# Performance work log

Hardware: AMD Instinct MI355X
Metric: run time of the kernel (lower is better)

## Reference

```python
import jax, jax.numpy as jnp
import numpy as np

D_K = 766  # feature dim, also softmax temperature per module init
NEG = -1000000000.0


def setup_inputs() -> dict:
    key = jax.random.key(0)
    k1, k2, k3 = jax.random.split(key, 3)
    B, H, L, D = 2, 4, 2048, D_K
    Q = jax.random.normal(k1, (B, H, L, D), dtype=jnp.float32)
    K = jax.random.normal(k2, (B, H, L, D), dtype=jnp.float32)
    attn_mask = jax.random.randint(k3, (B, H, L, L), 0, 2) > 0  # bool [B,H,Lk,Lq]
    return {"Q": Q, "K": K, "attn_mask": attn_mask}


def reference(Q, K, attn_mask):
    # scores: [B,H,Lq,Lk]
    scores = jnp.einsum("bhqd,bhkd->bhqk", Q, K) / np.sqrt(D_K).astype(np.float32)
    # mask is [B,H,Lk,Lq]; torch applies mask.transpose(2,3)
    scores = jnp.where(jnp.swapaxes(attn_mask, 2, 3), NEG, scores)
    attn1 = jax.nn.softmax(scores, axis=-1)                       # row softmax
    attn2 = jax.nn.softmax(jnp.swapaxes(scores, -1, -2), axis=-1)  # col softmax
    # dropout prob = 0.0 -> identity
    context1 = jnp.einsum("bhqk,bhkd->bhqd", attn1, K)
    context2 = jnp.einsum("bhkq,bhqd->bhkd", attn2, Q)
    return (context1, context2, attn1, attn2)
```

## Files before the change

kernel.cpp:

```cpp
#include <hip/hip_runtime.h>
#include <math.h>

#define L 2048
#define DK 766
#define DKP 768
#define NBH 8
#define NR (NBH * L)
#define NEGV -1000000000.0f

typedef __attribute__((ext_vector_type(8))) short bf16x8_t;
typedef __attribute__((ext_vector_type(4))) float f32x4_t;

#define LDT 72

typedef __attribute__((address_space(1))) const unsigned int gu32;
typedef __attribute__((address_space(3))) unsigned int lu32;

__device__ __forceinline__ short f2bf(float x) {
    union { float f; unsigned u; } v;
    v.f = x;
    unsigned r = v.u + 0x7fff + ((v.u >> 16) & 1);
    return (short)(r >> 16);
}

__device__ __forceinline__ float bf2f(short s) {
    union { unsigned u; float f; } v;
    v.u = ((unsigned)(unsigned short)s) << 16;
    return v.f;
}

__device__ __forceinline__ void gl_lds16(const void* g, void* l) {
    __builtin_amdgcn_global_load_lds((gu32*)g, (lu32*)l, 16, 0, 0);
}

#define BARR() asm volatile("s_barrier" ::: "memory")
#define VMW() asm volatile("s_waitcnt vmcnt(0)" ::: "memory")
#define PRIO1() __builtin_amdgcn_s_setprio(1)
#define PRIO0() __builtin_amdgcn_s_setprio(0)

__global__ __launch_bounds__(256) void k_cvtT(const float* __restrict__ Q,
                                              const float* __restrict__ K,
                                              short* __restrict__ Qb,
                                              short* __restrict__ Kb,
                                              short* __restrict__ Qt,
                                              short* __restrict__ Kt) {
    __shared__ short T[64 * LDT];
    const int tz = blockIdx.z;
    const int bh = tz & 7;
    const float* X = (tz < 8) ? Q : K;
    short* Xb = (tz < 8) ? Qb : Kb;
    short* Xt = (tz < 8) ? Qt : Kt;
    X += (size_t)bh * L * DK;
    Xb += (size_t)bh * L * DKP;
    Xt += (size_t)bh * DKP * L;
    const int r0 = blockIdx.y * 64, c0 = blockIdx.x * 64;
    const int t = threadIdx.x;
    const int rl = t >> 2, cc = (t & 3) * 16;

    bf16x8_t v0, v1;
#pragma unroll
    for (int p = 0; p < 8; ++p) {
        int c = c0 + cc + 2 * p;
        float2 f = (c < DK) ? *(const float2*)&X[(size_t)(r0 + rl) * DK + c]
                            : make_float2(0.f, 0.f);
        if (p < 4) { v0[2 * p] = f2bf(f.x); v0[2 * p + 1] = f2bf(f.y); }
        else { v1[2 * (p - 4)] = f2bf(f.x); v1[2 * (p - 4) + 1] = f2bf(f.y); }
    }
    *(bf16x8_t*)&Xb[(size_t)(r0 + rl) * DKP + c0 + cc] = v0;
    *(bf16x8_t*)&Xb[(size_t)(r0 + rl) * DKP + c0 + cc + 8] = v1;
    *(bf16x8_t*)&T[rl * LDT + cc] = v0;
    *(bf16x8_t*)&T[rl * LDT + cc + 8] = v1;
    __syncthreads();
    bf16x8_t w0, w1;
#pragma unroll
    for (int p = 0; p < 8; ++p) {
        w0[p] = T[(cc + p) * LDT + rl];
        w1[p] = T[(cc + 8 + p) * LDT + rl];
    }
    *(bf16x8_t*)&Xt[(size_t)(c0 + rl) * L + r0 + cc] = w0;
    *(bf16x8_t*)&Xt[(size_t)(c0 + rl) * L + r0 + cc + 8] = w1;
}

__global__ __launch_bounds__(256) void k_scoresT(const short* __restrict__ Kb,
                                                 const short* __restrict__ Qb,
                                                 const int* __restrict__ mask,
                                                 short* __restrict__ Sb,
                                                 float* __restrict__ prowM,
                                                 float* __restrict__ prowS,
                                                 float* __restrict__ pcolM,
                                                 float* __restrict__ pcolS) {
    __shared__ __align__(16) short As[128 * 64];
    __shared__ __align__(16) short Bs[128 * 64];
    int flat = blockIdx.x + (blockIdx.y << 4) + (blockIdx.z << 8);
    int nw = (flat & 7) * 256 + (flat >> 3);
    const int bxp = nw & 15;
    const int byp = (nw >> 4) & 15;
    const int bh = nw >> 8;

    const short* Am = Kb + (size_t)bh * L * DKP;
    const short* Bm = Qb + (size_t)bh * L * DKP;
    const int* Mm = mask + (size_t)bh * L * L;
    short* Sm = Sb + (size_t)bh * L * L;
    const int m0 = byp * 128, n0 = bxp * 128;
    const int t = threadIdx.x, lane = t & 63, wid = t >> 6;
    const int wm = (wid >> 1) * 64, wn = (wid & 1) * 64;
    const int lr = lane & 15, lg = lane >> 4;
    const int lrow = lane >> 3, lcol = lane & 7;

    f32x4_t acc[4][4];
#pragma unroll
    for (int i = 0; i < 4; ++i)
#pragma unroll
        for (int j = 0; j < 4; ++j) acc[i][j] = f32x4_t{0.f, 0.f, 0.f, 0.f};

    for (int k0 = 0; k0 < DKP; k0 += 64) {
#pragma unroll
        for (int g = 0; g < 4; ++g) {
            int row = wid * 32 + g * 8 + lrow;
            gl_lds16(&Am[(size_t)(m0 + row) * DKP + k0 + lcol * 8],
                     (char*)As + wid * 4096 + g * 1024);
            gl_lds16(&Bm[(size_t)(n0 + row) * DKP + k0 + lcol * 8],
                     (char*)Bs + wid * 4096 + g * 1024);
        }
        __syncthreads();
#pragma unroll
        for (int ks = 0; ks < 2; ++ks) {
            bf16x8_t av[4], bv[4];
#pragma unroll
            for (int i = 0; i < 4; ++i)
                av[i] = *(bf16x8_t*)&As[(wm + i * 16 + lr) * 64 + ks * 32 + lg * 8];
#pragma unroll
            for (int j = 0; j < 4; ++j)
                bv[j] = *(bf16x8_t*)&Bs[(wn + j * 16 + lr) * 64 + ks * 32 + lg * 8];
#pragma unroll
            for (int i = 0; i < 4; ++i)
#pragma unroll
                for (int j = 0; j < 4; ++j)
                    acc[i][j] = __builtin_amdgcn_mfma_f32_16x16x32_bf16(
                        av[i], bv[j], acc[i][j], 0, 0, 0);
        }
        __syncthreads();
    }

    const float scale = 1.0f / sqrtf((float)DK);
#pragma unroll
    for (int i = 0; i < 4; ++i) {
        int krow = m0 + wm + i * 16 + lg * 4;
#pragma unroll
        for (int j = 0; j < 4; ++j) {
            int qcol = n0 + wn + j * 16 + lr;
#pragma unroll
            for (int r = 0; r < 4; ++r) {
                int mv = Mm[(size_t)(krow + r) * L + qcol];
                float v = mv ? NEGV : acc[i][j][r] * scale;
                acc[i][j][r] = v;
                Sm[(size_t)(krow + r) * L + qcol] = f2bf(v);
            }
        }
    }

    float* redb = (float*)As;
#pragma unroll
    for (int i = 0; i < 4; ++i) {
#pragma unroll
        for (int r = 0; r < 4; ++r) {
            float rm = fmaxf(fmaxf(acc[i][0][r], acc[i][1][r]),
                             fmaxf(acc[i][2][r], acc[i][3][r]));
#pragma unroll
            for (int m = 1; m < 16; m <<= 1) rm = fmaxf(rm, __shfl_xor(rm, m, 64));
            float rs = 0.f;
#pragma unroll
            for (int j = 0; j < 4; ++j) rs += expf(acc[i][j][r] - rm);
#pragma unroll
            for (int m = 1; m < 16; m <<= 1) rs += __shfl_xor(rs, m, 64);
            if (lr == 0) {
                int row = wm + i * 16 + lg * 4 + r;
                redb[(wid & 1) * 128 + row] = rm;
                redb[256 + (wid & 1) * 128 + row] = rs;
            }
        }
    }
#pragma unroll
    for (int j = 0; j < 4; ++j) {
        float cm = -INFINITY;
#pragma unroll
        for (int i = 0; i < 4; ++i)
#pragma unroll
            for (int r = 0; r < 4; ++r) cm = fmaxf(cm, acc[i][j][r]);
        cm = fmaxf(cm, __shfl_xor(cm, 16, 64));
        cm = fmaxf(cm, __shfl_xor(cm, 32, 64));
        float cs = 0.f;
#pragma unroll
        for (int i = 0; i < 4; ++i)
#pragma unroll
            for (int r = 0; r < 4; ++r) cs += expf(acc[i][j][r] - cm);
        cs += __shfl_xor(cs, 16, 64);
        cs += __shfl_xor(cs, 32, 64);
        if (lg == 0) {
            int col = wn + j * 16 + lr;
            redb[512 + (wid >> 1) * 128 + col] = cm;
            redb[768 + (wid >> 1) * 128 + col] = cs;
        }
    }
    __syncthreads();
    if (t < 128) {
        float mA = redb[t], mB = redb[128 + t];
        float sA = redb[256 + t], sB = redb[256 + 128 + t];
        float mm = fmaxf(mA, mB);
        float ss = sA * expf(mA - mm) + sB * expf(mB - mm);
        size_t o = (size_t)bxp * NR + bh * L + m0 + t;
        prowM[o] = mm;
        prowS[o] = ss;
    } else {
        int c = t - 128;
        float mA = redb[512 + c], mB = redb[512 + 128 + c];
        float sA = redb[768 + c], sB = redb[768 + 128 + c];
        float mm = fmaxf(mA, mB);
        float ss = sA * expf(mA - mm) + sB * expf(mB - mm);
        size_t o = (size_t)byp * NR + bh * L + n0 + c;
        pcolM[o] = mm;
        pcolS[o] = ss;
    }
}

__global__ __launch_bounds__(256) void k_comb16(const float* __restrict__ prowM,
                                                const float* __restrict__ prowS,
                                                const float* __restrict__ pcolM,
                                                const float* __restrict__ pcolS,
                                                float* __restrict__ m1,
                                                float* __restrict__ r1,
                                                float* __restrict__ m2,
                                                float* __restrict__ r2) {
    int idx = blockIdx.x * 256 + threadIdx.x;
    float m = -INFINITY;
#pragma unroll
    for (int c = 0; c < 16; ++c) m = fmaxf(m, prowM[(size_t)c * NR + idx]);
    float s = 0.f;
#pragma unroll
    for (int c = 0; c < 16; ++c)
        s += prowS[(size_t)c * NR + idx] * expf(prowM[(size_t)c * NR + idx] - m);
    m2[idx] = m;
    r2[idx] = 1.0f / s;

    m = -INFINITY;
#pragma unroll
    for (int c = 0; c < 16; ++c) m = fmaxf(m, pcolM[(size_t)c * NR + idx]);
    s = 0.f;
#pragma unroll
    for (int c = 0; c < 16; ++c)
        s += pcolS[(size_t)c * NR + idx] * expf(pcolM[(size_t)c * NR + idx] - m);
    m1[idx] = m;
    r1[idx] = 1.0f / s;
}

__global__ __launch_bounds__(256) void k_apply(const short* __restrict__ Sb,
                                               const float* __restrict__ mr,
                                               const float* __restrict__ rr,
                                               const float* __restrict__ mc,
                                               const float* __restrict__ rc,
                                               float* __restrict__ OutIn,
                                               float* __restrict__ OutTr,
                                               short* __restrict__ bIn,
                                               short* __restrict__ bTr) {
    __shared__ float T[64][65];
    const int bh = blockIdx.z;
    const int rb0 = blockIdx.x * 64, cb0 = blockIdx.y * 64;
    const short* Sm = Sb + (size_t)bh * L * L;
    float* Oin = OutIn + (size_t)bh * L * L;
    float* Otr = OutTr + (size_t)bh * L * L;
    const int t = threadIdx.x, tx = t & 15, ty = t >> 4;

    float4 mcv = *(const float4*)&mc[bh * L + cb0 + tx * 4];
    float4 rcv = *(const float4*)&rc[bh * L + cb0 + tx * 4];

#pragma unroll
    for (int i = 0; i < 4; ++i) {
        int r = rb0 + ty * 4 + i;
        float mrv = mr[bh * L + r], rrv = rr[bh * L + r];
        short4 sx = *(const short4*)&Sm[(size_t)r * L + cb0 + tx * 4];
        float x0 = bf2f(sx.x), x1 = bf2f(sx.y), x2 = bf2f(sx.z), x3 = bf2f(sx.w);
        float4 e = make_float4(expf(x0 - mrv) * rrv, expf(x1 - mrv) * rrv,
                               expf(x2 - mrv) * rrv, expf(x3 - mrv) * rrv);
        *(float4*)&Oin[(size_t)r * L + cb0 + tx * 4] = e;
        short4 b = make_short4(f2bf(e.x), f2bf(e.y), f2bf(e.z), f2bf(e.w));
        *(short4*)&bIn[(size_t)bh * L * L + (size_t)r * L + cb0 + tx * 4] = b;
        T[tx * 4 + 0][ty * 4 + i] = expf(x0 - mcv.x) * rcv.x;
        T[tx * 4 + 1][ty * 4 + i] = expf(x1 - mcv.y) * rcv.y;
        T[tx * 4 + 2][ty * 4 + i] = expf(x2 - mcv.z) * rcv.z;
        T[tx * 4 + 3][ty * 4 + i] = expf(x3 - mcv.w) * rcv.w;
    }
    __syncthreads();
#pragma unroll
    for (int i = 0; i < 4; ++i) {
        int c = ty * 4 + i;
        float4 v = make_float4(T[c][tx * 4], T[c][tx * 4 + 1], T[c][tx * 4 + 2],
                               T[c][tx * 4 + 3]);
        *(float4*)&Otr[(size_t)(cb0 + c) * L + rb0 + tx * 4] = v;
        short4 b = make_short4(f2bf(v.x), f2bf(v.y), f2bf(v.z), f2bf(v.w));
        *(short4*)&bTr[(size_t)bh * L * L + (size_t)(cb0 + c) * L + rb0 + tx * 4] = b;
    }
}

__global__ __launch_bounds__(512, 2) void k_ctx8(const short* __restrict__ a1b,
                                                 const short* __restrict__ a2b,
                                                 const short* __restrict__ Kt,
                                                 const short* __restrict__ Qt,
                                                 float* __restrict__ c1,
                                                 float* __restrict__ c2) {
    __shared__ __align__(16) short LB[57344];

    int flat = blockIdx.x;
    int nw = (flat & 7) * 64 + (flat >> 3);
    int inst = nw >> 5, rem = nw & 31;
    int myp = rem >> 2, nxp = rem & 3;
    int bh = inst & 7;
    const short* Am = ((inst < 8) ? a1b : a2b) + (size_t)bh * L * L;
    const short* Bt = ((inst < 8) ? Kt : Qt) + (size_t)bh * DKP * L;
    float* Cm = ((inst < 8) ? c1 : c2) + (size_t)bh * L * DK;
    const int m0 = myp * 256, n0 = nxp * 192;

    const int t = threadIdx.x, lane = t & 63, wid = t >> 6;
    const int wr = wid >> 2, wc = wid & 3;
    const int lr = lane & 15, lg = lane >> 4;

    const int schunk = (lane & 7) ^ (lane >> 3);
    const short* aSrc = Am + (size_t)(m0 + wid * 8 + (lane >> 3)) * L + schunk * 8;
    const short* bSrc = Bt + (size_t)(n0 + wid * 8 + (lane >> 3)) * L + schunk * 8;
    char* ldsA = (char*)LB;
    char* ldsB = (char*)LB + 65536;

#define STAGEA(cb, k0n)                                                               \
    do {                                                                              \
        gl_lds16(aSrc + (k0n), ldsA + (cb)*32768 + wid * 1024);                       \
        gl_lds16(aSrc + (size_t)64 * L + (k0n), ldsA + (cb)*32768 + 8192 + wid * 1024); \
        gl_lds16(aSrc + (size_t)128 * L + (k0n), ldsA + (cb)*32768 + 16384 + wid * 1024); \
        gl_lds16(aSrc + (size_t)192 * L + (k0n), ldsA + (cb)*32768 + 24576 + wid * 1024); \
    } while (0)
#define STAGEB(cb, k0n)                                                               \
    do {                                                                              \
        gl_lds16(bSrc + (k0n), ldsB + (cb)*24576 + wid * 1024);                       \
        gl_lds16(bSrc + (size_t)64 * L + (k0n), ldsB + (cb)*24576 + 8192 + wid * 1024); \
        gl_lds16(bSrc + (size_t)128 * L + (k0n), ldsB + (cb)*24576 + 16384 + wid * 1024); \
    } while (0)

    const int axr = lr & 7;
    const int kc0 = ((0 + lg) ^ axr) * 8;
    const int kc1 = ((4 + lg) ^ axr) * 8;
    const int aRd = wr * 8192 + lr * 64;
    const int bRd = 32768 + (wc * 48 + lr) * 64;

#define LDA0(c, i) (*(const bf16x8_t*)&LB[(c)*16384 + aRd + (i)*1024 + kc0])
#define LDA1(c, i) (*(const bf16x8_t*)&LB[(c)*16384 + aRd + (i)*1024 + kc1])
#define LDB0(c, j) (*(const bf16x8_t*)&LB[bRd + (c)*12288 + (j)*1024 + kc0])
#define LDB1(c, j) (*(const bf16x8_t*)&LB[bRd + (c)*12288 + (j)*1024 + kc1])

    f32x4_t acc[8][3];
#pragma unroll
    for (int i = 0; i < 8; ++i)
#pragma unroll
        for (int j = 0; j < 3; ++j) acc[i][j] = f32x4_t{0.f, 0.f, 0.f, 0.f};

    bf16x8_t bfr[3][2];

#define PHASE(c, i0, EXTRA)                                                           \
    do {                                                                              \
        bf16x8_t a00 = LDA0(c, i0), a01 = LDA1(c, i0);                                \
        bf16x8_t a10 = LDA0(c, (i0) + 1), a11 = LDA1(c, (i0) + 1);                    \
        EXTRA;                                                                        \
        BARR();                                                                       \
        PRIO1();                                                                      \
        _Pragma("unroll") for (int j = 0; j < 3; ++j) {                               \
            acc[i0][j] = __builtin_amdgcn_mfma_f32_16x16x32_bf16(a00, bfr[j][0],      \
                                                                 acc[i0][j], 0, 0, 0); \
            acc[i0][j] = __builtin_amdgcn_mfma_f32_16x16x32_bf16(a01, bfr[j][1],      \
                                                                 acc[i0][j], 0, 0, 0); \
            acc[(i0) + 1][j] = __builtin_amdgcn_mfma_f32_16x16x32_bf16(               \
                a10, bfr[j][0], acc[(i0) + 1][j], 0, 0, 0);                           \
            acc[(i0) + 1][j] = __builtin_amdgcn_mfma_f32_16x16x32_bf16(               \
                a11, bfr[j][1], acc[(i0) + 1][j], 0, 0, 0);                           \
        }                                                                             \
        PRIO0();                                                                      \
    } while (0)

    const int NT = L / 64;
    STAGEA(0, 0);
    STAGEB(0, 0);
    VMW();
    BARR();

    for (int kt = 0; kt < NT; ++kt) {
        const int c = kt & 1;
        const bool ds = (kt + 1 < NT);
        const int k0n = (kt + 1) * 64;
#pragma unroll
        for (int j = 0; j < 3; ++j) {
            bfr[j][0] = LDB0(c, j);
            bfr[j][1] = LDB1(c, j);
        }
        PHASE(c, 0, if (ds) STAGEA(c ^ 1, k0n));
        BARR();
        PHASE(c, 2, if (ds) STAGEB(c ^ 1, k0n));
        BARR();
        PHASE(c, 4, ((void)0));
        BARR();
        PHASE(c, 6, ((void)0));
        if (ds) VMW();
        BARR();
    }

#pragma unroll
    for (int i = 0; i < 8; ++i) {
        int row = m0 + wr * 128 + i * 16 + lg * 4;
#pragma unroll
        for (int j = 0; j < 3; ++j) {
            int col = n0 + wc * 48 + j * 16 + lr;
            if (col < DK) {
#pragma unroll
                for (int r = 0; r < 4; ++r)
                    Cm[(size_t)(row + r) * DK + col] = acc[i][j][r];
            }
        }
    }
#undef PHASE
#undef STAGEA
#undef STAGEB
#undef LDA0
#undef LDA1
#undef LDB0
#undef LDB1
}

extern "C" void kernel_launch(void* const* d_in, const int* in_sizes, int n_in,
                              void* d_out, int out_size, void* d_ws, size_t ws_size,
                              hipStream_t stream) {
    const float* Q = (const float*)d_in[0];
    const float* K = (const float*)d_in[1];
    const int* mask = (const int*)d_in[2];
    float* out = (float*)d_out;

    const size_t CTX = (size_t)NBH * L * DK;
    const size_t ATT = (size_t)NBH * L * L;
    float* c1 = out;
    float* c2 = out + CTX;
    float* a1 = out + 2 * CTX;
    float* a2 = out + 2 * CTX + ATT;

    float* ws = (float*)d_ws;
    float* m1 = ws;
    float* r1 = ws + NR;
    float* m2 = ws + 2 * (size_t)NR;
    float* r2 = ws + 3 * (size_t)NR;
    const size_t QBE = (size_t)NBH * L * DKP;
    short* Qb = (short*)(ws + 4 * (size_t)NR);
    short* Kb = Qb + QBE;
    short* a1b = Kb + QBE;
    short* a2b = a1b + ATT;
    short* Qt = a2b + ATT;
    short* Kt = Qt + QBE;

    float* prowM = c1;
    float* prowS = c1 + 16 * (size_t)NR;
    float* pcolM = c1 + 32 * (size_t)NR;
    float* pcolS = c1 + 48 * (size_t)NR;

    dim3 blk(256);

    k_cvtT<<<dim3(12, 32, 16), blk, 0, stream>>>(Q, K, Qb, Kb, Qt, Kt);
    k_scoresT<<<dim3(16, 16, NBH), blk, 0, stream>>>(Kb, Qb, mask, a2b, prowM, prowS,
                                                     pcolM, pcolS);
    k_comb16<<<dim3(NR / 256), blk, 0, stream>>>(prowM, prowS, pcolM, pcolS, m1, r1,
                                                 m2, r2);
    k_apply<<<dim3(32, 32, NBH), blk, 0, stream>>>(a2b, m2, r2, m1, r1, a2, a1, a2b,
                                                   a1b);
    k_ctx8<<<dim3(512), dim3(512), 0, stream>>>(a1b, a2b, Kt, Qt, c1, c2);
}
```

Baseline: 448.1 us.

## Enlarge score tiles to 256x256 with double-buffered swizzled LDS pipeline

Replaces the 128x128 score GEMM kernel with a 512-thread kernel computing 256x256 tiles, double-buffering K/Q chunks in 128KB LDS with XOR-swizzled layout and interleaving global-to-LDS staging with MFMA phases. Larger tiles halve the operand reload traffic and the number of partial softmax statistics, so the combine kernel now reduces 8 partials instead of 16. The cost is higher register and LDS use per block, which limits occupancy, and it relies on barrier/priority helper macros defined elsewhere in the file.

Measured after the change: 431.8 us (median of 2 runs). 3.6% less time.

```diff
diff --git a/kernel.cpp b/kernel.cpp
--- a/kernel.cpp
+++ b/kernel.cpp
@@ -81,74 +81,123 @@
     *(bf16x8_t*)&Xt[(size_t)(c0 + rl) * L + r0 + cc + 8] = w1;
 }
 
-__global__ __launch_bounds__(256) void k_scoresT(const short* __restrict__ Kb,
-                                                 const short* __restrict__ Qb,
-                                                 const int* __restrict__ mask,
-                                                 short* __restrict__ Sb,
-                                                 float* __restrict__ prowM,
-                                                 float* __restrict__ prowS,
-                                                 float* __restrict__ pcolM,
-                                                 float* __restrict__ pcolS) {
-    __shared__ __align__(16) short As[128 * 64];
-    __shared__ __align__(16) short Bs[128 * 64];
-    int flat = blockIdx.x + (blockIdx.y << 4) + (blockIdx.z << 8);
-    int nw = (flat & 7) * 256 + (flat >> 3);
-    const int bxp = nw & 15;
-    const int byp = (nw >> 4) & 15;
-    const int bh = nw >> 8;
-
+__global__ __launch_bounds__(512, 2) void k_score8(const short* __restrict__ Kb,
+                                                   const short* __restrict__ Qb,
+                                                   const int* __restrict__ mask,
+                                                   short* __restrict__ Sb,
+                                                   float* __restrict__ prowM,
+                                                   float* __restrict__ prowS,
+                                                   float* __restrict__ pcolM,
+                                                   float* __restrict__ pcolS) {
+    __shared__ __align__(16) short LB[65536];
+
+    int flat = blockIdx.x;
+    int nw = (flat & 7) * 64 + (flat >> 3);
+    int bh = nw >> 6, rem = nw & 63;
+    int byp = rem >> 3, bxp = rem & 7;
     const short* Am = Kb + (size_t)bh * L * DKP;
     const short* Bm = Qb + (size_t)bh * L * DKP;
     const int* Mm = mask + (size_t)bh * L * L;
     short* Sm = Sb + (size_t)bh * L * L;
-    const int m0 = byp * 128, n0 = bxp * 128;
+    const int m0 = byp * 256, n0 = bxp * 256;
+
     const int t = threadIdx.x, lane = t & 63, wid = t >> 6;
-    const int wm = (wid >> 1) * 64, wn = (wid & 1) * 64;
+    const int wr = wid >> 2, wc = wid & 3;
     const int lr = lane & 15, lg = lane >> 4;
-    const int lrow = lane >> 3, lcol = lane & 7;
-
-    f32x4_t acc[4][4];
-#pragma unroll
-    for (int i = 0; i < 4; ++i)
+
+    const int schunk = (lane & 7) ^ (lane >> 3);
+    const short* aSrc = Am + (size_t)(m0 + wid * 8 + (lane >> 3)) * DKP + schunk * 8;
+    const short* bSrc = Bm + (size_t)(n0 + wid * 8 + (lane >> 3)) * DKP + schunk * 8;
+    char* ldsA = (char*)LB;
+    char* ldsB = (char*)LB + 65536;
+
+#define STAGEA(cb, k0n)                                                                 \
+    do {                                                                                \
+        gl_lds16(aSrc + (k0n), ldsA + (cb)*32768 + wid * 1024);                         \
+        gl_lds16(aSrc + (size_t)64 * DKP + (k0n), ldsA + (cb)*32768 + 8192 + wid * 1024);  \
+        gl_lds16(aSrc + (size_t)128 * DKP + (k0n), ldsA + (cb)*32768 + 16384 + wid * 1024); \
+        gl_lds16(aSrc + (size_t)192 * DKP + (k0n), ldsA + (cb)*32768 + 24576 + wid * 1024); \
+    } while (0)
+#define STAGEB(cb, k0n)                                                                 \
+    do {                                                                                \
+        gl_lds16(bSrc + (k0n), ldsB + (cb)*32768 + wid * 1024);                         \
+        gl_lds16(bSrc + (size_t)64 * DKP + (k0n), ldsB + (cb)*32768 + 8192 + wid * 1024);  \
+        gl_lds16(bSrc + (size_t)128 * DKP + (k0n), ldsB + (cb)*32768 + 16384 + wid * 1024); \
+        gl_lds16(bSrc + (size_t)192 * DKP + (k0n), ldsB + (cb)*32768 + 24576 + wid * 1024); \
+    } while (0)
+
+    const int axr = lr & 7;
+    const int kc0 = ((0 + lg) ^ axr) * 8;
+    const int kc1 = ((4 + lg) ^ axr) * 8;
+    const int aRd = wr * 8192 + lr * 64;
+    const int bRd = 32768 + (wc >> 1) * 8192 + ((wc & 1) * 64 + lr) * 64;
+
+#define LDA0(c, i) (*(const bf16x8_t*)&LB[(c)*16384 + aRd + (i)*1024 + kc0])
+#define LDA1(c, i) (*(const bf16x8_t*)&LB[(c)*16384 + aRd + (i)*1024 + kc1])
+#define LDB0(c, j) (*(const bf16x8_t*)&LB[(c)*16384 + bRd + (j)*1024 + kc0])
+#define LDB1(c, j) (*(const bf16x8_t*)&LB[(c)*16384 + bRd + (j)*1024 + kc1])
+
+    f32x4_t acc[8][4];
+#pragma unroll
+    for (int i = 0; i < 8; ++i)
 #pragma unroll
         for (int j = 0; j < 4; ++j) acc[i][j] = f32x4_t{0.f, 0.f, 0.f, 0.f};
 
-    for (int k0 = 0; k0 < DKP; k0 += 64) {
-#pragma unroll
-        for (int g = 0; g < 4; ++g) {
-            int row = wid * 32 + g * 8 + lrow;
-            gl_lds16(&Am[(size_t)(m0 + row) * DKP + k0 + lcol * 8],
-                     (char*)As + wid * 4096 + g * 1024);
-            gl_lds16(&Bm[(size_t)(n0 + row) * DKP + k0 + lcol * 8],
-                     (char*)Bs + wid * 4096 + g * 1024);
+    bf16x8_t bfr[4][2];
+
+#define PHASE(c, i0, EXTRA)                                                             \
+    do {                                                                                \
+        bf16x8_t a00 = LDA0(c, i0), a01 = LDA1(c, i0);                                  \
+        bf16x8_t a10 = LDA0(c, (i0) + 1), a11 = LDA1(c, (i0) + 1);                      \
+        EXTRA;                                                                          \
+        BARR();                                                                         \
+        PRIO1();                                                                        \
+        _Pragma("unroll") for (int j = 0; j < 4; ++j) {                                 \
+            acc[i0][j] = __builtin_amdgcn_mfma_f32_16x16x32_bf16(a00, bfr[j][0],        \
+                                                                 acc[i0][j], 0, 0, 0);  \
+            acc[i0][j] = __builtin_amdgcn_mfma_f32_16x16x32_bf16(a01, bfr[j][1],        \
+                                                                 acc[i0][j], 0, 0, 0);  \
+            acc[(i0) + 1][j] = __builtin_amdgcn_mfma_f32_16x16x32_bf16(                 \
+                a10, bfr[j][0], acc[(i0) + 1][j], 0, 0, 0);                             \
+            acc[(i0) + 1][j] = __builtin_amdgcn_mfma_f32_16x16x32_bf16(                 \
+                a11, bfr[j][1], acc[(i0) + 1][j], 0, 0, 0);                             \
+        }                                                                               \
+        PRIO0();                                                                        \
+    } while (0)
+
+    const int NT = DKP / 64;
+    STAGEA(0, 0);
+    STAGEB(0, 0);
+    VMW();
+    BARR();
+
+    for (int kt = 0; kt < NT; ++kt) {
+        const int c = kt & 1;
+        const bool ds = (kt + 1 < NT);
+        const int k0n = (kt + 1) * 64;
+#pragma unroll
+        for (int j = 0; j < 4; ++j) {
+            bfr[j][0] = LDB0(c, j);
+            bfr[j][1] = LDB1(c, j);
         }
-        __syncthreads();
-#pragma unroll
-        for (int ks = 0; ks < 2; ++ks) {
-            bf16x8_t av[4], bv[4];
-#pragma unroll
-            for (int i = 0; i < 4; ++i)
-                av[i] = *(bf16x8_t*)&As[(wm + i * 16 + lr) * 64 + ks * 32 + lg * 8];
-#pragma unroll
-            for (int j = 0; j < 4; ++j)
-                bv[j] = *(bf16x8_t*)&Bs[(wn + j * 16 + lr) * 64 + ks * 32 + lg * 8];
-#pragma unroll
-            for (int i = 0; i < 4; ++i)
-#pragma unroll
-                for (int j = 0; j < 4; ++j)
-                    acc[i][j] = __builtin_amdgcn_mfma_f32_16x16x32_bf16(
-                        av[i], bv[j], acc[i][j], 0, 0, 0);
-        }
-        __syncthreads();
+        PHASE(c, 0, if (ds) STAGEA(c ^ 1, k0n));
+        BARR();
+        PHASE(c, 2, if (ds) STAGEB(c ^ 1, k0n));
+        BARR();
+        PHASE(c, 4, ((void)0));
+        BARR();
+        PHASE(c, 6, ((void)0));
+        if (ds) VMW();
+        BARR();
     }
 
     const float scale = 1.0f / sqrtf((float)DK);
 #pragma unroll
-    for (int i = 0; i < 4; ++i) {
-        int krow = m0 + wm + i * 16 + lg * 4;
+    for (int i = 0; i < 8; ++i) {
+        int krow = m0 + wr * 128 + i * 16 + lg * 4;
 #pragma unroll
         for (int j = 0; j < 4; ++j) {
-            int qcol = n0 + wn + j * 16 + lr;
+            int qcol = n0 + wc * 64 + j * 16 + lr;
 #pragma unroll
             for (int r = 0; r < 4; ++r) {
                 int mv = Mm[(size_t)(krow + r) * L + qcol];
@@ -159,9 +208,11 @@
         }
     }
 
-    float* redb = (float*)As;
-#pragma unroll
-    for (int i = 0; i < 4; ++i) {
+    __syncthreads();
+    float* redb = (float*)LB;
+
+#pragma unroll
+    for (int i = 0; i < 8; ++i) {
 #pragma unroll
         for (int r = 0; r < 4; ++r) {
             float rm = fmaxf(fmaxf(acc[i][0][r], acc[i][1][r]),
@@ -174,9 +225,9 @@
 #pragma unroll
             for (int m = 1; m < 16; m <<= 1) rs += __shfl_xor(rs, m, 64);
             if (lr == 0) {
-                int row = wm + i * 16 + lg * 4 + r;
-                redb[(wid & 1) * 128 + row] = rm;
-                redb[256 + (wid & 1) * 128 + row] = rs;
+                int kr = wr * 128 + i * 16 + lg * 4 + r;
+                redb[wc * 256 + kr] = rm;
+                redb[1024 + wc * 256 + kr] = rs;
             }
         }
     }
@@ -184,70 +235,80 @@
     for (int j = 0; j < 4; ++j) {
         float cm = -INFINITY;
 #pragma unroll
-        for (int i = 0; i < 4; ++i)
+        for (int i = 0; i < 8; ++i)
 #pragma unroll
             for (int r = 0; r < 4; ++r) cm = fmaxf(cm, acc[i][j][r]);
         cm = fmaxf(cm, __shfl_xor(cm, 16, 64));
         cm = fmaxf(cm, __shfl_xor(cm, 32, 64));
         float cs = 0.f;
 #pragma unroll
-        for (int i = 0; i < 4; ++i)
+        for (int i = 0; i < 8; ++i)
 #pragma unroll
             for (int r = 0; r < 4; ++r) cs += expf(acc[i][j][r] - cm);
         cs += __shfl_xor(cs, 16, 64);
         cs += __shfl_xor(cs, 32, 64);
         if (lg == 0) {
-            int col = wn + j * 16 + lr;
-            redb[512 + (wid >> 1) * 128 + col] = cm;
-            redb[768 + (wid >> 1) * 128 + col] = cs;
+            int qc = wc * 64 + j * 16 + lr;
+            redb[2048 + wr * 256 + qc] = cm;
+            redb[2560 + wr * 256 + qc] = cs;
         }
     }
     __syncthreads();
-    if (t < 128) {
-        float mA = redb[t], mB = redb[128 + t];
-        float sA = redb[256 + t], sB = redb[256 + 128 + t];
-        float mm = fmaxf(mA, mB);
-        float ss = sA * expf(mA - mm) + sB * expf(mB - mm);
+    if (t < 256) {
+        float m = redb[t];
+        float s = 0.f;
+#pragma unroll
+        for (int w = 1; w < 4; ++w) m = fmaxf(m, redb[w * 256 + t]);
+#pragma unroll
+        for (int w = 0; w < 4; ++w)
+            s += redb[1024 + w * 256 + t] * expf(redb[w * 256 + t] - m);
         size_t o = (size_t)bxp * NR + bh * L + m0 + t;
-        prowM[o] = mm;
-        prowS[o] = ss;
+        prowM[o] = m;
+        prowS[o] = s;
     } else {
-        int c = t - 128;
-        float mA = redb[512 + c], mB = redb[512 + 128 + c];
-        float sA = redb[768 + c], sB = redb[768 + 128 + c];
-        float mm = fmaxf(mA, mB);
-        float ss = sA * expf(mA - mm) + sB * expf(mB - mm);
-        size_t o = (size_t)byp * NR + bh * L + n0 + c;
-        pcolM[o] = mm;
-        pcolS[o] = ss;
-    }
-}
-
-__global__ __launch_bounds__(256) void k_comb16(const float* __restrict__ prowM,
-                                                const float* __restrict__ prowS,
-                                                const float* __restrict__ pcolM,
-                                                const float* __restrict__ pcolS,
-                                                float* __restrict__ m1,
-                                                float* __restrict__ r1,
-                                                float* __restrict__ m2,
-                                                float* __restrict__ r2) {
+        int qc = t - 256;
+        float mA = redb[2048 + qc], mB = redb[2048 + 256 + qc];
+        float sA = redb[2560 + qc], sB = redb[2560 + 256 + qc];
+        float m = fmaxf(mA, mB);
+        float s = sA * expf(mA - m) + sB * expf(mB - m);
+        size_t o = (size_t)byp * NR + bh * L + n0 + qc;
+        pcolM[o] = m;
+        pcolS[o] = s;
+    }
+#undef PHASE
+#undef STAGEA
+#undef STAGEB
+#undef LDA0
+#undef LDA1
+#undef LDB0
+#undef LDB1
+}
+
+__global__ __launch_bounds__(256) void k_comb8(const float* __restrict__ prowM,
+                                               const float* __restrict__ prowS,
+                                               const float* __restrict__ pcolM,
+                                               const float* __restrict__ pcolS,
+                                               float* __restrict__ m1,
+                                               float* __restrict__ r1,
+                                               float* __restrict__ m2,
+                                               float* __restrict__ r2) {
     int idx = blockIdx.x * 256 + threadIdx.x;
     float m = -INFINITY;
 #pragma unroll
-    for (int c = 0; c < 16; ++c) m = fmaxf(m, prowM[(size_t)c * NR + idx]);
+    for (int c = 0; c < 8; ++c) m = fmaxf(m, prowM[(size_t)c * NR + idx]);
     float s = 0.f;
 #pragma unroll
-    for (int c = 0; c < 16; ++c)
+    for (int c = 0; c < 8; ++c)
         s += prowS[(size_t)c * NR + idx] * expf(prowM[(size_t)c * NR + idx] - m);
     m2[idx] = m;
     r2[idx] = 1.0f / s;
 
     m = -INFINITY;
 #pragma unroll
-    for (int c = 0; c < 16; ++c) m = fmaxf(m, pcolM[(size_t)c * NR + idx]);
+    for (int c = 0; c < 8; ++c) m = fmaxf(m, pcolM[(size_t)c * NR + idx]);
     s = 0.f;
 #pragma unroll
-    for (int c = 0; c < 16; ++c)
+    for (int c = 0; c < 8; ++c)
         s += pcolS[(size_t)c * NR + idx] * expf(pcolM[(size_t)c * NR + idx] - m);
     m1[idx] = m;
     r1[idx] = 1.0f / s;
@@ -459,17 +520,17 @@
     short* Kt = Qt + QBE;
 
     float* prowM = c1;
-    float* prowS = c1 + 16 * (size_t)NR;
-    float* pcolM = c1 + 32 * (size_t)NR;
-    float* pcolS = c1 + 48 * (size_t)NR;
+    float* prowS = c1 + 8 * (size_t)NR;
+    float* pcolM = c1 + 16 * (size_t)NR;
+    float* pcolS = c1 + 24 * (size_t)NR;
 
     dim3 blk(256);
 
     k_cvtT<<<dim3(12, 32, 16), blk, 0, stream>>>(Q, K, Qb, Kb, Qt, Kt);
-    k_scoresT<<<dim3(16, 16, NBH), blk, 0, stream>>>(Kb, Qb, mask, a2b, prowM, prowS,
-                                                     pcolM, pcolS);
-    k_comb16<<<dim3(NR / 256), blk, 0, stream>>>(prowM, prowS, pcolM, pcolS, m1, r1,
-                                                 m2, r2);
+    k_score8<<<dim3(512), dim3(512), 0, stream>>>(Kb, Qb, mask, a2b, prowM, prowS,
+                                                  pcolM, pcolS);
+    k_comb8<<<dim3(NR / 256), blk, 0, stream>>>(prowM, prowS, pcolM, pcolS, m1, r1,
+                                                m2, r2);
     k_apply<<<dim3(32, 32, NBH), blk, 0, stream>>>(a2b, m2, r2, m1, r1, a2, a1, a2b,
                                                    a1b);
     k_ctx8<<<dim3(512), dim3(512), 0, stream>>>(a1b, a2b, Kt, Qt, c1, c2);
```

## Enlarge score GEMM tile to 256x128 with 512 threads and swizzled LDS

Applied to the files above, without the earlier changes.

Rewrites the score kernel to use 256x128 output tiles with 8 waves per block, an XOR-swizzled LDS layout to avoid bank conflicts, and scheduling-priority hints around the MFMA loop. The column-partial count drops from 16 to 8, which the combine kernel and the workspace offsets now reflect. The aim is more operand reuse per loaded tile, fewer LDS bank conflicts, and less partial-reduction traffic. The trade-off is higher register and LDS pressure per block. The macros VMW, BARR and PRIO are assumed to be defined in the part of the file not shown.

New measurement: 411.2 us, median of 2. 8.2% less time.

```diff
diff --git a/kernel.cpp b/kernel.cpp
--- a/kernel.cpp
+++ b/kernel.cpp
@@ -81,31 +81,39 @@
     *(bf16x8_t*)&Xt[(size_t)(c0 + rl) * L + r0 + cc + 8] = w1;
 }
 
-__global__ __launch_bounds__(256) void k_scoresT(const short* __restrict__ Kb,
-                                                 const short* __restrict__ Qb,
-                                                 const int* __restrict__ mask,
-                                                 short* __restrict__ Sb,
-                                                 float* __restrict__ prowM,
-                                                 float* __restrict__ prowS,
-                                                 float* __restrict__ pcolM,
-                                                 float* __restrict__ pcolS) {
-    __shared__ __align__(16) short As[128 * 64];
-    __shared__ __align__(16) short Bs[128 * 64];
-    int flat = blockIdx.x + (blockIdx.y << 4) + (blockIdx.z << 8);
-    int nw = (flat & 7) * 256 + (flat >> 3);
-    const int bxp = nw & 15;
-    const int byp = (nw >> 4) & 15;
-    const int bh = nw >> 8;
-
+__global__ __launch_bounds__(512, 4) void k_score2(const short* __restrict__ Kb,
+                                                   const short* __restrict__ Qb,
+                                                   const int* __restrict__ mask,
+                                                   short* __restrict__ Sb,
+                                                   float* __restrict__ prowM,
+                                                   float* __restrict__ prowS,
+                                                   float* __restrict__ pcolM,
+                                                   float* __restrict__ pcolS) {
+    __shared__ __align__(16) short LB[24576];
+
+    int flat = blockIdx.x;
+    int nw = (flat & 7) * 128 + (flat >> 3);
+    int bh = nw >> 7, rem = nw & 127;
+    int byp = rem >> 4, bxp = rem & 15;
     const short* Am = Kb + (size_t)bh * L * DKP;
     const short* Bm = Qb + (size_t)bh * L * DKP;
     const int* Mm = mask + (size_t)bh * L * L;
     short* Sm = Sb + (size_t)bh * L * L;
-    const int m0 = byp * 128, n0 = bxp * 128;
+    const int m0 = byp * 256, n0 = bxp * 128;
+
     const int t = threadIdx.x, lane = t & 63, wid = t >> 6;
-    const int wm = (wid >> 1) * 64, wn = (wid & 1) * 64;
+    const int wr = wid >> 1, wc = wid & 1;
     const int lr = lane & 15, lg = lane >> 4;
-    const int lrow = lane >> 3, lcol = lane & 7;
+
+    const int schunk = (lane & 7) ^ (lane >> 3);
+    const short* aSrc = Am + (size_t)(m0 + wid * 32 + (lane >> 3)) * DKP + schunk * 8;
+    const short* bSrc = Bm + (size_t)(n0 + wid * 16 + (lane >> 3)) * DKP + schunk * 8;
+    char* ldsA = (char*)LB;
+    char* ldsB = (char*)LB + 32768;
+
+    const int axr = lr & 7;
+    const int kc0 = ((0 + lg) ^ axr) * 8;
+    const int kc1 = ((4 + lg) ^ axr) * 8;
 
     f32x4_t acc[4][4];
 #pragma unroll
@@ -113,25 +121,28 @@
 #pragma unroll
         for (int j = 0; j < 4; ++j) acc[i][j] = f32x4_t{0.f, 0.f, 0.f, 0.f};
 
-    for (int k0 = 0; k0 < DKP; k0 += 64) {
-#pragma unroll
-        for (int g = 0; g < 4; ++g) {
-            int row = wid * 32 + g * 8 + lrow;
-            gl_lds16(&Am[(size_t)(m0 + row) * DKP + k0 + lcol * 8],
-                     (char*)As + wid * 4096 + g * 1024);
-            gl_lds16(&Bm[(size_t)(n0 + row) * DKP + k0 + lcol * 8],
-                     (char*)Bs + wid * 4096 + g * 1024);
-        }
-        __syncthreads();
+    const int NT = DKP / 64;
+    for (int kt = 0; kt < NT; ++kt) {
+        const int k0 = kt * 64;
+#pragma unroll
+        for (int g = 0; g < 4; ++g)
+            gl_lds16(aSrc + (size_t)(8 * g) * DKP + k0, ldsA + wid * 4096 + g * 1024);
+#pragma unroll
+        for (int g = 0; g < 2; ++g)
+            gl_lds16(bSrc + (size_t)(8 * g) * DKP + k0, ldsB + wid * 2048 + g * 1024);
+        VMW();
+        BARR();
+        PRIO1();
 #pragma unroll
         for (int ks = 0; ks < 2; ++ks) {
+            const int kc = ks ? kc1 : kc0;
             bf16x8_t av[4], bv[4];
 #pragma unroll
             for (int i = 0; i < 4; ++i)
-                av[i] = *(bf16x8_t*)&As[(wm + i * 16 + lr) * 64 + ks * 32 + lg * 8];
+                av[i] = *(const bf16x8_t*)&LB[wr * 4096 + i * 1024 + lr * 64 + kc];
 #pragma unroll
             for (int j = 0; j < 4; ++j)
-                bv[j] = *(bf16x8_t*)&Bs[(wn + j * 16 + lr) * 64 + ks * 32 + lg * 8];
+                bv[j] = *(const bf16x8_t*)&LB[16384 + wc * 4096 + j * 1024 + lr * 64 + kc];
 #pragma unroll
             for (int i = 0; i < 4; ++i)
 #pragma unroll
@@ -139,16 +150,17 @@
                     acc[i][j] = __builtin_amdgcn_mfma_f32_16x16x32_bf16(
                         av[i], bv[j], acc[i][j], 0, 0, 0);
         }
-        __syncthreads();
+        PRIO0();
+        BARR();
     }
 
     const float scale = 1.0f / sqrtf((float)DK);
 #pragma unroll
     for (int i = 0; i < 4; ++i) {
-        int krow = m0 + wm + i * 16 + lg * 4;
+        int krow = m0 + wr * 64 + i * 16 + lg * 4;
 #pragma unroll
         for (int j = 0; j < 4; ++j) {
-            int qcol = n0 + wn + j * 16 + lr;
+            int qcol = n0 + wc * 64 + j * 16 + lr;
 #pragma unroll
             for (int r = 0; r < 4; ++r) {
                 int mv = Mm[(size_t)(krow + r) * L + qcol];
@@ -159,7 +171,9 @@
         }
     }
 
-    float* redb = (float*)As;
+    __syncthreads();
+    float* redb = (float*)LB;
+
 #pragma unroll
     for (int i = 0; i < 4; ++i) {
 #pragma unroll
@@ -174,9 +188,9 @@
 #pragma unroll
             for (int m = 1; m < 16; m <<= 1) rs += __shfl_xor(rs, m, 64);
             if (lr == 0) {
-                int row = wm + i * 16 + lg * 4 + r;
-                redb[(wid & 1) * 128 + row] = rm;
-                redb[256 + (wid & 1) * 128 + row] = rs;
+                int kr = wr * 64 + i * 16 + lg * 4 + r;
+                redb[wc * 256 + kr] = rm;
+                redb[512 + wc * 256 + kr] = rs;
             }
         }
     }
@@ -197,40 +211,43 @@
         cs += __shfl_xor(cs, 16, 64);
         cs += __shfl_xor(cs, 32, 64);
         if (lg == 0) {
-            int col = wn + j * 16 + lr;
-            redb[512 + (wid >> 1) * 128 + col] = cm;
-            redb[768 + (wid >> 1) * 128 + col] = cs;
+            int qc = wc * 64 + j * 16 + lr;
+            redb[1024 + wr * 128 + qc] = cm;
+            redb[1536 + wr * 128 + qc] = cs;
         }
     }
     __syncthreads();
-    if (t < 128) {
-        float mA = redb[t], mB = redb[128 + t];
-        float sA = redb[256 + t], sB = redb[256 + 128 + t];
-        float mm = fmaxf(mA, mB);
-        float ss = sA * expf(mA - mm) + sB * expf(mB - mm);
+    if (t < 256) {
+        float mA = redb[t], mB = redb[256 + t];
+        float sA = redb[512 + t], sB = redb[512 + 256 + t];
+        float m = fmaxf(mA, mB);
+        float s = sA * expf(mA - m) + sB * expf(mB - m);
         size_t o = (size_t)bxp * NR + bh * L + m0 + t;
-        prowM[o] = mm;
-        prowS[o] = ss;
-    } else {
-        int c = t - 128;
-        float mA = redb[512 + c], mB = redb[512 + 128 + c];
-        float sA = redb[768 + c], sB = redb[768 + 128 + c];
-        float mm = fmaxf(mA, mB);
-        float ss = sA * expf(mA - mm) + sB * expf(mB - mm);
-        size_t o = (size_t)byp * NR + bh * L + n0 + c;
-        pcolM[o] = mm;
-        pcolS[o] = ss;
-    }
-}
-
-__global__ __launch_bounds__(256) void k_comb16(const float* __restrict__ prowM,
-                                                const float* __restrict__ prowS,
-                                                const float* __restrict__ pcolM,
-                                                const float* __restrict__ pcolS,
-                                                float* __restrict__ m1,
-                                                float* __restrict__ r1,
-                                                float* __restrict__ m2,
-                                                float* __restrict__ r2) {
+        prowM[o] = m;
+        prowS[o] = s;
+    } else if (t < 384) {
+        int qc = t - 256;
+        float m = redb[1024 + qc];
+#pragma unroll
+        for (int w = 1; w < 4; ++w) m = fmaxf(m, redb[1024 + w * 128 + qc]);
+        float s = 0.f;
+#pragma unroll
+        for (int w = 0; w < 4; ++w)
+            s += redb[1536 + w * 128 + qc] * expf(redb[1024 + w * 128 + qc] - m);
+        size_t o = (size_t)byp * NR + bh * L + n0 + qc;
+        pcolM[o] = m;
+        pcolS[o] = s;
+    }
+}
+
+__global__ __launch_bounds__(256) void k_comb(const float* __restrict__ prowM,
+                                              const float* __restrict__ prowS,
+                                              const float* __restrict__ pcolM,
+                                              const float* __restrict__ pcolS,
+                                              float* __restrict__ m1,
+                                              float* __restrict__ r1,
+                                              float* __restrict__ m2,
+                                              float* __restrict__ r2) {
     int idx = blockIdx.x * 256 + threadIdx.x;
     float m = -INFINITY;
 #pragma unroll
@@ -244,10 +261,10 @@
 
     m = -INFINITY;
 #pragma unroll
-    for (int c = 0; c < 16; ++c) m = fmaxf(m, pcolM[(size_t)c * NR + idx]);
+    for (int c = 0; c < 8; ++c) m = fmaxf(m, pcolM[(size_t)c * NR + idx]);
     s = 0.f;
 #pragma unroll
-    for (int c = 0; c < 16; ++c)
+    for (int c = 0; c < 8; ++c)
         s += pcolS[(size_t)c * NR + idx] * expf(pcolM[(size_t)c * NR + idx] - m);
     m1[idx] = m;
     r1[idx] = 1.0f / s;
@@ -461,15 +478,15 @@
     float* prowM = c1;
     float* prowS = c1 + 16 * (size_t)NR;
     float* pcolM = c1 + 32 * (size_t)NR;
-    float* pcolS = c1 + 48 * (size_t)NR;
+    float* pcolS = c1 + 40 * (size_t)NR;
 
     dim3 blk(256);
 
     k_cvtT<<<dim3(12, 32, 16), blk, 0, stream>>>(Q, K, Qb, Kb, Qt, Kt);
-    k_scoresT<<<dim3(16, 16, NBH), blk, 0, stream>>>(Kb, Qb, mask, a2b, prowM, prowS,
-                                                     pcolM, pcolS);
-    k_comb16<<<dim3(NR / 256), blk, 0, stream>>>(prowM, prowS, pcolM, pcolS, m1, r1,
-                                                 m2, r2);
+    k_score2<<<dim3(1024), dim3(512), 0, stream>>>(Kb, Qb, mask, a2b, prowM, prowS,
+                                                   pcolM, pcolS);
+    k_comb<<<dim3(NR / 256), blk, 0, stream>>>(prowM, prowS, pcolM, pcolS, m1, r1,
+                                               m2, r2);
     k_apply<<<dim3(32, 32, NBH), blk, 0, stream>>>(a2b, m2, r2, m1, r1, a2, a1, a2b,
                                                    a1b);
     k_ctx8<<<dim3(512), dim3(512), 0, stream>>>(a1b, a2b, Kt, Qt, c1, c2);
```
